# Kernel optimization log

Measured on AMD Instinct MI355X. Metric: run time of the kernel, lower is better.

Reference implementation:

```python
import jax, jax.numpy as jnp
import numpy as np
from jax import lax

D_MODEL = 1024
STATE_DIM = 512
BATCH = 4
SEQ_LEN = 8192


def _cayley_eigenvalues(a_params, n):
    # a_full = [0, a_1..a_half, -a_half-1..., antisymmetric tail]
    half = n // 2
    a_full = jnp.zeros((n,), dtype=a_params.dtype)
    a_full = a_full.at[1:half + 1].set(a_params)
    a_full = a_full.at[half + 1:].set(-a_params[::-1][: n - half - 1])
    a_hat = jnp.fft.fft(a_full)            # complex64
    omega = jnp.imag(a_hat)                # (n,), float32
    ones = jnp.ones_like(omega)
    num = lax.complex(ones, -omega)
    den = lax.complex(ones, omega)
    return num / den                        # (n,), |lambda|=1


def setup_inputs() -> dict:
    key = jax.random.key(0)
    k1, k2, k3, k4 = jax.random.split(key, 4)
    u = jax.random.normal(k1, (BATCH, SEQ_LEN, D_MODEL), dtype=jnp.float32)
    a_params = jax.random.normal(k2, (STATE_DIM // 2,), dtype=jnp.float32) * 0.1
    # torch Linear weights: B.weight (state_dim, d_model), C.weight (d_model, state_dim)
    B_w = jax.random.normal(k3, (STATE_DIM, D_MODEL), dtype=jnp.float32) / np.sqrt(D_MODEL)
    C_w = jax.random.normal(k4, (D_MODEL, STATE_DIM), dtype=jnp.float32) / np.sqrt(STATE_DIM)
    D = jnp.ones((D_MODEL,), dtype=jnp.float32)
    return {"u": u, "a_params": a_params, "B_w": B_w, "C_w": C_w, "D": D}


def reference(u, a_params, B_w, C_w, D):
    batch, seq_len, d = u.shape
    n = B_w.shape[0]
    # 1) input projection: (b, t, n)
    Bu = jnp.einsum("btd,nd->btn", u, B_w)
    # 2) per-channel geometric kernel k_j[t] = lambda_j^t
    eig = _cayley_eigenvalues(a_params, n)                 # (n,) complex64
    t = jnp.arange(seq_len, dtype=jnp.float32)
    kernel = jnp.exp(t[:, None] * jnp.log(eig)[None, :])   # (T, n) complex64
    # 3) causal convolution via FFT with next-pow2(2T) padding
    fft_len = 1
    while fft_len < 2 * seq_len:
        fft_len *= 2
    pad = fft_len - seq_len
    kernel_padded = jnp.pad(kernel, ((0, pad), (0, 0)))
    K_hat = jnp.fft.fft(kernel_padded, axis=0)             # (F, n)
    Bu_padded = jnp.pad(Bu, ((0, 0), (0, pad), (0, 0))).astype(jnp.complex64)
    Bu_hat = jnp.fft.fft(Bu_padded, axis=1)                # (b, F, n)
    h = jnp.fft.ifft(K_hat[None] * Bu_hat, axis=1).real[:, :seq_len, :]
    # 4) output projection + skip
    y = jnp.einsum("btn,dn->btd", h, C_w) + D * u
    return y
```

## Files before the change

### kernel.cpp

```cpp
#include <hip/hip_runtime.h>
#include <cstdint>
#include <cstddef>

#define D_MODEL   1024
#define STATE_DIM 512
#define BATCH     4
#define SEQ_LEN   8192
#define M_TOTAL   (BATCH * SEQ_LEN)

typedef unsigned short ushort_t;
typedef __attribute__((ext_vector_type(8))) __bf16 bf16x8;
typedef __attribute__((ext_vector_type(4))) float  f32x4;


__device__ inline ushort_t f2bf(float f) {
  union { float f; uint32_t u; } v; v.f = f;
  uint32_t u = v.u;
  uint32_t r = (u + 0x7FFFu + ((u >> 16) & 1u)) >> 16;
  return (ushort_t)r;
}

__device__ inline float bf2f(ushort_t b) {
  union { uint32_t u; float f; } v; v.u = ((uint32_t)b) << 16;
  return v.f;
}

__device__ inline void llds16(const void* g, void* l) {
  __builtin_amdgcn_global_load_lds(
      (__attribute__((address_space(1))) void*)(void*)g,
      (__attribute__((address_space(3))) void*)l,
      16, 0, 0);
}


__global__ void convert_f32_bf16(const float* __restrict__ in,
                                 ushort_t* __restrict__ out, int n4) {
  int i = blockIdx.x * blockDim.x + threadIdx.x;
  if (i >= n4) return;
  const float4 v = ((const float4*)in)[i];
  ushort4 o;
  o.x = f2bf(v.x); o.y = f2bf(v.y); o.z = f2bf(v.z); o.w = f2bf(v.w);
  ((ushort4*)out)[i] = o;
}


__global__ __launch_bounds__(64)
void eigen_kernel(const float* __restrict__ a_params, float* __restrict__ lam) {
  const int k = blockIdx.x;
  const int l = threadIdx.x;
  const float c = 6.283185307179586f / 512.0f;
  float om = 0.f;
#pragma unroll
  for (int s = 0; s < 8; ++s) {
    const int n = s * 64 + l;
    float v = 0.f;
    if (n >= 1 && n <= STATE_DIM / 2)      v = a_params[n - 1];
    else if (n > STATE_DIM / 2)            v = -a_params[STATE_DIM - n];
    const int p = (k * n) & 511;
    om -= v * sinf(c * (float)p);
  }
#pragma unroll
  for (int off = 32; off; off >>= 1) om += __shfl_down(om, off);
  if (l == 0) {
    const float d  = 1.f / (1.f + om * om);
    const float lr = (1.f - om * om) * d;
    const float li = -2.f * om * d;
    double th = atan2((double)li, (double)lr) * 128.0;
    lam[k]        = lr;
    lam[512 + k]  = li;
    lam[1024 + k] = (float)cos(th);
    lam[1536 + k] = (float)sin(th);
  }
}


template <int KDIM, int NDIM, bool OUT_BF16, bool FUSE_SKIP>
__global__ __launch_bounds__(256, 4)
void gemm_bt(const ushort_t* __restrict__ A,
             const ushort_t* __restrict__ Bw,
             void* __restrict__ outv,
             const ushort_t* __restrict__ skip_b,
             const float* __restrict__ Dvec) {
  __shared__ __align__(16) ushort_t smA[128 * 32];
  __shared__ __align__(16) ushort_t smB[128 * 32];
  const int tid    = threadIdx.x;
  const int wave   = tid >> 6, lane = tid & 63;
  const int lane16 = lane & 15, quad = lane >> 4;
  const int wm = (wave & 1) * 64, wn = (wave >> 1) * 64;
  const int row0 = blockIdx.x * 128;
  const int col0 = blockIdx.y * 128;

  f32x4 acc[4][4];
#pragma unroll
  for (int i = 0; i < 4; ++i)
#pragma unroll
    for (int j = 0; j < 4; ++j) {
      f32x4 z = {0.f, 0.f, 0.f, 0.f};
      acc[i][j] = z;
    }

  const int s_r0 = tid >> 2;
  const int s_c0 = (tid & 3) ^ ((s_r0 >> 1) & 3);
  const int s_r1 = (256 + tid) >> 2;
  const int s_c1 = (tid & 3) ^ ((s_r1 >> 1) & 3);

  for (int k0 = 0; k0 < KDIM; k0 += 32) {
    {
      const ushort_t* gA0 = A  + (size_t)(row0 + s_r0) * KDIM + k0 + s_c0 * 8;
      const ushort_t* gB0 = Bw + (size_t)(col0 + s_r0) * KDIM + k0 + s_c0 * 8;
      const ushort_t* gA1 = A  + (size_t)(row0 + s_r1) * KDIM + k0 + s_c1 * 8;
      const ushort_t* gB1 = Bw + (size_t)(col0 + s_r1) * KDIM + k0 + s_c1 * 8;
      const int o0 = (wave * 64) * 16;
      const int o1 = (256 + wave * 64) * 16;
      llds16(gA0, (char*)smA + o0);
      llds16(gB0, (char*)smB + o0);
      llds16(gA1, (char*)smA + o1);
      llds16(gB1, (char*)smB + o1);
    }
    __syncthreads();

    bf16x8 af[4], bfr[4];
#pragma unroll
    for (int mi = 0; mi < 4; ++mi) {
      const int m = wm + mi * 16 + lane16;
      const int pc = quad ^ ((m >> 1) & 3);
      af[mi] = *(const bf16x8*)(smA + (m * 4 + pc) * 8);
    }
#pragma unroll
    for (int ni = 0; ni < 4; ++ni) {
      const int n = wn + ni * 16 + lane16;
      const int pc = quad ^ ((n >> 1) & 3);
      bfr[ni] = *(const bf16x8*)(smB + (n * 4 + pc) * 8);
    }
#pragma unroll
    for (int mi = 0; mi < 4; ++mi)
#pragma unroll
      for (int ni = 0; ni < 4; ++ni)
        acc[mi][ni] = __builtin_amdgcn_mfma_f32_16x16x32_bf16(
            af[mi], bfr[ni], acc[mi][ni], 0, 0, 0);
    __syncthreads();
  }

#pragma unroll
  for (int mi = 0; mi < 4; ++mi) {
#pragma unroll
    for (int ni = 0; ni < 4; ++ni) {
      const int row = row0 + wm + mi * 16 + quad * 4;
      const int col = col0 + wn + ni * 16 + lane16;
      float dv = 0.f;
      if (FUSE_SKIP) dv = Dvec[col];
#pragma unroll
      for (int r = 0; r < 4; ++r) {
        const size_t o = (size_t)(row + r) * NDIM + col;
        float val = acc[mi][ni][r];
        if (FUSE_SKIP) val = fmaf(dv, bf2f(skip_b[o]), val);
        if (OUT_BF16) ((ushort_t*)outv)[o] = f2bf(val);
        else          ((float*)outv)[o] = val;
      }
    }
  }
}


#define NCHUNK 64
#define CLEN   128
#define SOFF   (BATCH * NCHUNK * STATE_DIM)

__global__ __launch_bounds__(512)
void scan_chunks(const ushort_t* __restrict__ Bu, const float* __restrict__ lam,
                 float* __restrict__ S) {
  const int j = threadIdx.x;
  const int c = blockIdx.x & (NCHUNK - 1);
  const int b = blockIdx.x >> 6;
  const float lr = lam[j], li = lam[512 + j];
  const ushort_t* p = Bu + ((size_t)(b * SEQ_LEN + c * CLEN)) * STATE_DIM + j;
  float hr = 0.f, hi = 0.f;
#pragma unroll 4
  for (int t = 0; t < CLEN; ++t) {
    const float x  = bf2f(p[(size_t)t * STATE_DIM]);
    const float nr = fmaf(lr, hr, fmaf(-li, hi, x));
    const float ni = fmaf(lr, hi, li * hr);
    hr = nr; hi = ni;
  }
  const size_t o = (size_t)(b * NCHUNK + c) * STATE_DIM + j;
  S[o] = hr; S[SOFF + o] = hi;
}

__global__ __launch_bounds__(512)
void scan_carry(const float* __restrict__ lam, const float* __restrict__ S,
                float* __restrict__ Hin) {
  const int idx = blockIdx.x * blockDim.x + threadIdx.x;
  const int j = idx & 511, b = idx >> 9;
  const float pr = lam[1024 + j], pi = lam[1536 + j];
  float cr = 0.f, ci = 0.f;
  for (int c = 0; c < NCHUNK; ++c) {
    const size_t o = (size_t)(b * NCHUNK + c) * STATE_DIM + j;
    Hin[o] = cr; Hin[SOFF + o] = ci;
    const float sr = S[o], si = S[SOFF + o];
    const float nr = fmaf(pr, cr, fmaf(-pi, ci, sr));
    const float ni = fmaf(pr, ci, fmaf(pi, cr, si));
    cr = nr; ci = ni;
  }
}

__global__ __launch_bounds__(512)
void scan_final(const ushort_t* __restrict__ Bu, const float* __restrict__ lam,
                const float* __restrict__ Hin, ushort_t* __restrict__ h) {
  const int j = threadIdx.x;
  const int c = blockIdx.x & (NCHUNK - 1);
  const int b = blockIdx.x >> 6;
  const float lr = lam[j], li = lam[512 + j];
  const size_t so = (size_t)(b * NCHUNK + c) * STATE_DIM + j;
  float hr = Hin[so], hi = Hin[SOFF + so];
  const size_t base = ((size_t)(b * SEQ_LEN + c * CLEN)) * STATE_DIM + j;
#pragma unroll 4
  for (int t = 0; t < CLEN; ++t) {
    const float x  = bf2f(Bu[base + (size_t)t * STATE_DIM]);
    const float nr = fmaf(lr, hr, fmaf(-li, hi, x));
    const float ni = fmaf(lr, hi, li * hr);
    hr = nr; hi = ni;
    h[base + (size_t)t * STATE_DIM] = f2bf(hr);
  }
}


extern "C" void kernel_launch(void* const* d_in, const int* in_sizes, int n_in,
                              void* d_out, int out_size, void* d_ws, size_t ws_size,
                              hipStream_t stream) {
  const float* u  = (const float*)d_in[0];
  const float* ap = (const float*)d_in[1];
  const float* Bw = (const float*)d_in[2];
  const float* Cw = (const float*)d_in[3];
  const float* Dv = (const float*)d_in[4];
  float* y = (float*)d_out;

  char* ws = (char*)d_ws;
  ushort_t* ub  = (ushort_t*)(ws + 0);
  ushort_t* bwb = (ushort_t*)(ws + 67108864);
  ushort_t* cwb = (ushort_t*)(ws + 68157440);
  float*    lam = (float*)   (ws + 69206016);
  ushort_t* Bu  = (ushort_t*)(ws + 69214208);
  ushort_t* hb  = (ushort_t*)(ws + 102768640);
  float*    S   = (float*)   (ws + 136323072);
  float*    Hin = (float*)   (ws + 137371648);

  convert_f32_bf16<<<32768, 256, 0, stream>>>(u,  ub,  (M_TOTAL * D_MODEL) / 4);
  convert_f32_bf16<<<512,   256, 0, stream>>>(Bw, bwb, (STATE_DIM * D_MODEL) / 4);
  convert_f32_bf16<<<512,   256, 0, stream>>>(Cw, cwb, (D_MODEL * STATE_DIM) / 4);
  eigen_kernel<<<512, 64, 0, stream>>>(ap, lam);

  gemm_bt<D_MODEL, STATE_DIM, true, false>
      <<<dim3(M_TOTAL / 128, STATE_DIM / 128), 256, 0, stream>>>(
          ub, bwb, Bu, nullptr, nullptr);

  scan_chunks<<<BATCH * NCHUNK, 512, 0, stream>>>(Bu, lam, S);
  scan_carry<<<BATCH, 512, 0, stream>>>(lam, S, Hin);
  scan_final<<<BATCH * NCHUNK, 512, 0, stream>>>(Bu, lam, Hin, hb);

  gemm_bt<STATE_DIM, D_MODEL, false, true>
      <<<dim3(M_TOTAL / 128, D_MODEL / 128), 256, 0, stream>>>(
          hb, cwb, y, ub, Dv);
}
```

Before: 392.5 us.

## Double-buffer GEMM LDS loads and vectorize chunked scan with shorter chunks

The GEMM now double-buffers its shared-memory tiles, issuing the async global-to-LDS load for the next K slice while MFMAs run on the current one. This cuts the sync stalls per iteration and doubles the LDS footprint. The scan changes to 128 chunks of 64 steps, and each thread handles 4 adjacent state channels with 4-wide bf16 loads and stores, giving more blocks and wider memory transactions. The carry scan now walks twice as many chunks serially, and the workspace offset for Hin moves to fit the larger S buffer.

```diff
diff --git a/kernel.cpp b/kernel.cpp
--- a/kernel.cpp
+++ b/kernel.cpp
@@ -44,6 +44,10 @@
 }
 
 
+#define NCHUNK 128
+#define CLEN   64
+#define SOFF   (BATCH * NCHUNK * STATE_DIM)
+
 __global__ __launch_bounds__(64)
 void eigen_kernel(const float* __restrict__ a_params, float* __restrict__ lam) {
   const int k = blockIdx.x;
@@ -65,7 +69,7 @@
     const float d  = 1.f / (1.f + om * om);
     const float lr = (1.f - om * om) * d;
     const float li = -2.f * om * d;
-    double th = atan2((double)li, (double)lr) * 128.0;
+    double th = atan2((double)li, (double)lr) * (double)CLEN;
     lam[k]        = lr;
     lam[512 + k]  = li;
     lam[1024 + k] = (float)cos(th);
@@ -81,8 +85,8 @@
              void* __restrict__ outv,
              const ushort_t* __restrict__ skip_b,
              const float* __restrict__ Dvec) {
-  __shared__ __align__(16) ushort_t smA[128 * 32];
-  __shared__ __align__(16) ushort_t smB[128 * 32];
+  __shared__ __align__(16) ushort_t smA[2 * 128 * 32];
+  __shared__ __align__(16) ushort_t smB[2 * 128 * 32];
   const int tid    = threadIdx.x;
   const int wave   = tid >> 6, lane = tid & 63;
   const int lane16 = lane & 15, quad = lane >> 4;
@@ -103,34 +107,47 @@
   const int s_c0 = (tid & 3) ^ ((s_r0 >> 1) & 3);
   const int s_r1 = (256 + tid) >> 2;
   const int s_c1 = (tid & 3) ^ ((s_r1 >> 1) & 3);
-
-  for (int k0 = 0; k0 < KDIM; k0 += 32) {
-    {
-      const ushort_t* gA0 = A  + (size_t)(row0 + s_r0) * KDIM + k0 + s_c0 * 8;
-      const ushort_t* gB0 = Bw + (size_t)(col0 + s_r0) * KDIM + k0 + s_c0 * 8;
-      const ushort_t* gA1 = A  + (size_t)(row0 + s_r1) * KDIM + k0 + s_c1 * 8;
-      const ushort_t* gB1 = Bw + (size_t)(col0 + s_r1) * KDIM + k0 + s_c1 * 8;
-      const int o0 = (wave * 64) * 16;
-      const int o1 = (256 + wave * 64) * 16;
-      llds16(gA0, (char*)smA + o0);
-      llds16(gB0, (char*)smB + o0);
-      llds16(gA1, (char*)smA + o1);
-      llds16(gB1, (char*)smB + o1);
-    }
-    __syncthreads();
-
+  const int o0 = (wave * 64) * 16;
+  const int o1 = (256 + wave * 64) * 16;
+
+  const ushort_t* gA0 = A  + (size_t)(row0 + s_r0) * KDIM + s_c0 * 8;
+  const ushort_t* gB0 = Bw + (size_t)(col0 + s_r0) * KDIM + s_c0 * 8;
+  const ushort_t* gA1 = A  + (size_t)(row0 + s_r1) * KDIM + s_c1 * 8;
+  const ushort_t* gB1 = Bw + (size_t)(col0 + s_r1) * KDIM + s_c1 * 8;
+
+#define STAGE(k0, buf)                                                   \
+  do {                                                                   \
+    char* bA = (char*)(smA + (buf) * (128 * 32));                        \
+    char* bB = (char*)(smB + (buf) * (128 * 32));                        \
+    llds16(gA0 + (k0), bA + o0);                                         \
+    llds16(gB0 + (k0), bB + o0);                                         \
+    llds16(gA1 + (k0), bA + o1);                                         \
+    llds16(gB1 + (k0), bB + o1);                                         \
+  } while (0)
+
+  STAGE(0, 0);
+  __syncthreads();
+
+  constexpr int NIT = KDIM / 32;
+  int cur = 0;
+#pragma unroll 2
+  for (int it = 0; it < NIT; ++it) {
+    if (it + 1 < NIT) STAGE((it + 1) * 32, cur ^ 1);
+
+    const ushort_t* sA = smA + cur * (128 * 32);
+    const ushort_t* sB = smB + cur * (128 * 32);
     bf16x8 af[4], bfr[4];
 #pragma unroll
     for (int mi = 0; mi < 4; ++mi) {
       const int m = wm + mi * 16 + lane16;
       const int pc = quad ^ ((m >> 1) & 3);
-      af[mi] = *(const bf16x8*)(smA + (m * 4 + pc) * 8);
+      af[mi] = *(const bf16x8*)(sA + (m * 4 + pc) * 8);
     }
 #pragma unroll
     for (int ni = 0; ni < 4; ++ni) {
       const int n = wn + ni * 16 + lane16;
       const int pc = quad ^ ((n >> 1) & 3);
-      bfr[ni] = *(const bf16x8*)(smB + (n * 4 + pc) * 8);
+      bfr[ni] = *(const bf16x8*)(sB + (n * 4 + pc) * 8);
     }
 #pragma unroll
     for (int mi = 0; mi < 4; ++mi)
@@ -138,8 +155,11 @@
       for (int ni = 0; ni < 4; ++ni)
         acc[mi][ni] = __builtin_amdgcn_mfma_f32_16x16x32_bf16(
             af[mi], bfr[ni], acc[mi][ni], 0, 0, 0);
+
     __syncthreads();
-  }
+    cur ^= 1;
+  }
+#undef STAGE
 
 #pragma unroll
   for (int mi = 0; mi < 4; ++mi) {
@@ -162,28 +182,30 @@
 }
 
 
-#define NCHUNK 64
-#define CLEN   128
-#define SOFF   (BATCH * NCHUNK * STATE_DIM)
-
-__global__ __launch_bounds__(512)
+__global__ __launch_bounds__(128)
 void scan_chunks(const ushort_t* __restrict__ Bu, const float* __restrict__ lam,
                  float* __restrict__ S) {
-  const int j = threadIdx.x;
+  const int j = threadIdx.x * 4;
   const int c = blockIdx.x & (NCHUNK - 1);
-  const int b = blockIdx.x >> 6;
-  const float lr = lam[j], li = lam[512 + j];
+  const int b = blockIdx.x >> 7;
+  float lr[4], li[4], hr[4] = {0,0,0,0}, hi[4] = {0,0,0,0};
+#pragma unroll
+  for (int q = 0; q < 4; ++q) { lr[q] = lam[j + q]; li[q] = lam[512 + j + q]; }
   const ushort_t* p = Bu + ((size_t)(b * SEQ_LEN + c * CLEN)) * STATE_DIM + j;
-  float hr = 0.f, hi = 0.f;
 #pragma unroll 4
   for (int t = 0; t < CLEN; ++t) {
-    const float x  = bf2f(p[(size_t)t * STATE_DIM]);
-    const float nr = fmaf(lr, hr, fmaf(-li, hi, x));
-    const float ni = fmaf(lr, hi, li * hr);
-    hr = nr; hi = ni;
+    const ushort4 x4 = *(const ushort4*)(p + (size_t)t * STATE_DIM);
+    const float x[4] = {bf2f(x4.x), bf2f(x4.y), bf2f(x4.z), bf2f(x4.w)};
+#pragma unroll
+    for (int q = 0; q < 4; ++q) {
+      const float nr = fmaf(lr[q], hr[q], fmaf(-li[q], hi[q], x[q]));
+      const float ni = fmaf(lr[q], hi[q], li[q] * hr[q]);
+      hr[q] = nr; hi[q] = ni;
+    }
   }
   const size_t o = (size_t)(b * NCHUNK + c) * STATE_DIM + j;
-  S[o] = hr; S[SOFF + o] = hi;
+#pragma unroll
+  for (int q = 0; q < 4; ++q) { S[o + q] = hr[q]; S[SOFF + o + q] = hi[q]; }
 }
 
 __global__ __launch_bounds__(512)
@@ -203,23 +225,32 @@
   }
 }
 
-__global__ __launch_bounds__(512)
+__global__ __launch_bounds__(128)
 void scan_final(const ushort_t* __restrict__ Bu, const float* __restrict__ lam,
                 const float* __restrict__ Hin, ushort_t* __restrict__ h) {
-  const int j = threadIdx.x;
+  const int j = threadIdx.x * 4;
   const int c = blockIdx.x & (NCHUNK - 1);
-  const int b = blockIdx.x >> 6;
-  const float lr = lam[j], li = lam[512 + j];
+  const int b = blockIdx.x >> 7;
+  float lr[4], li[4], hr[4], hi[4];
+#pragma unroll
+  for (int q = 0; q < 4; ++q) { lr[q] = lam[j + q]; li[q] = lam[512 + j + q]; }
   const size_t so = (size_t)(b * NCHUNK + c) * STATE_DIM + j;
-  float hr = Hin[so], hi = Hin[SOFF + so];
+#pragma unroll
+  for (int q = 0; q < 4; ++q) { hr[q] = Hin[so + q]; hi[q] = Hin[SOFF + so + q]; }
   const size_t base = ((size_t)(b * SEQ_LEN + c * CLEN)) * STATE_DIM + j;
 #pragma unroll 4
   for (int t = 0; t < CLEN; ++t) {
-    const float x  = bf2f(Bu[base + (size_t)t * STATE_DIM]);
-    const float nr = fmaf(lr, hr, fmaf(-li, hi, x));
-    const float ni = fmaf(lr, hi, li * hr);
-    hr = nr; hi = ni;
-    h[base + (size_t)t * STATE_DIM] = f2bf(hr);
+    const ushort4 x4 = *(const ushort4*)(Bu + base + (size_t)t * STATE_DIM);
+    const float x[4] = {bf2f(x4.x), bf2f(x4.y), bf2f(x4.z), bf2f(x4.w)};
+    ushort4 o4;
+#pragma unroll
+    for (int q = 0; q < 4; ++q) {
+      const float nr = fmaf(lr[q], hr[q], fmaf(-li[q], hi[q], x[q]));
+      const float ni = fmaf(lr[q], hi[q], li[q] * hr[q]);
+      hr[q] = nr; hi[q] = ni;
+    }
+    o4.x = f2bf(hr[0]); o4.y = f2bf(hr[1]); o4.z = f2bf(hr[2]); o4.w = f2bf(hr[3]);
+    *(ushort4*)(h + base + (size_t)t * STATE_DIM) = o4;
   }
 }
 
@@ -242,7 +273,7 @@
   ushort_t* Bu  = (ushort_t*)(ws + 69214208);
   ushort_t* hb  = (ushort_t*)(ws + 102768640);
   float*    S   = (float*)   (ws + 136323072);
-  float*    Hin = (float*)   (ws + 137371648);
+  float*    Hin = (float*)   (ws + 138420224);
 
   convert_f32_bf16<<<32768, 256, 0, stream>>>(u,  ub,  (M_TOTAL * D_MODEL) / 4);
   convert_f32_bf16<<<512,   256, 0, stream>>>(Bw, bwb, (STATE_DIM * D_MODEL) / 4);
@@ -253,9 +284,9 @@
       <<<dim3(M_TOTAL / 128, STATE_DIM / 128), 256, 0, stream>>>(
           ub, bwb, Bu, nullptr, nullptr);
 
-  scan_chunks<<<BATCH * NCHUNK, 512, 0, stream>>>(Bu, lam, S);
+  scan_chunks<<<BATCH * NCHUNK, 128, 0, stream>>>(Bu, lam, S);
   scan_carry<<<BATCH, 512, 0, stream>>>(lam, S, Hin);
-  scan_final<<<BATCH * NCHUNK, 512, 0, stream>>>(Bu, lam, Hin, hb);
+  scan_final<<<BATCH * NCHUNK, 128, 0, stream>>>(Bu, lam, Hin, hb);
 
   gemm_bt<STATE_DIM, D_MODEL, false, true>
       <<<dim3(M_TOTAL / 128, D_MODEL / 128), 256, 0, stream>>>(
```

New measurement: 374.6 us. 1.05x faster.
